# Performance work log

Measured on AMD Instinct MI355X. Metric: run time of the kernel, lower is better.

The kernel has to match this reference:

```python
import jax, jax.numpy as jnp
import numpy as np

N, M, FDIM, EDIM, H, HEADS = 8192, 8192, 128, 128, 64, 4
NEG = -1e9


def setup_inputs() -> dict:
    key = jax.random.key(0)
    ks = jax.random.split(key, 6)
    F0 = jax.random.normal(ks[0], (N, FDIM), dtype=jnp.float32)
    E0 = jax.random.normal(ks[1], (M, EDIM), dtype=jnp.float32)
    A = jax.random.randint(ks[2], (N, M), 0, 2, dtype=jnp.int32)
    Wf = jax.random.normal(ks[3], (HEADS, FDIM, H), dtype=jnp.float32) * 0.05
    We = jax.random.normal(ks[4], (HEADS, EDIM, H), dtype=jnp.float32) * 0.05
    a = jax.random.normal(ks[5], (HEADS, H), dtype=jnp.float32) * 0.05
    return {"F0": F0, "E0": E0, "A": A, "Wf": Wf, "We": We, "a": a}


def reference(F0, E0, A, Wf, We, a):
    # Per-head linear projections: h=head, n/m=nodes, d=hidden
    F1 = jnp.einsum('nf,hfd->hnd', F0, Wf)   # [H, N, D]
    E1 = jnp.einsum('me,hed->hmd', E0, We)   # [H, M, D]
    # Additive GAT scores: (h_src @ a) + (h_dst @ a), broadcast over the grid
    e_src = jnp.einsum('hnd,hd->hn', F1, a)  # [H, N]
    e_dst = jnp.einsum('hmd,hd->hm', E1, a)  # [H, M]
    e = jax.nn.leaky_relu(e_src[:, :, None] + e_dst[:, None, :], negative_slope=0.2)
    e = jnp.where(A[None, :, :] > 0, e, NEG)
    alpha = jax.nn.softmax(e, axis=-1)       # [H, N, M]
    h_prime = jnp.einsum('hnm,hmd->hnd', alpha, E1)  # [H, N, D]
    out = jnp.mean(h_prime, axis=0)          # mean over heads -> [N, D]
    return jax.nn.softmax(out, axis=-1)
```

## Files before the change

kernel.cpp:

```cpp
#include <hip/hip_runtime.h>
#include <hip/hip_fp16.h>

#define NN 8192
#define MM 8192
#define FD 128
#define EDm 128
#define HD 64
#define NH 4

#define MSPLIT 4
#define MRANGE (MM / MSPLIT)
#define MSTEP 128
#define NITER (MRANGE / MSTEP)
#define NTILE 32
#define AMS 132

typedef float f32x4 __attribute__((ext_vector_type(4)));
typedef _Float16 h16x8 __attribute__((ext_vector_type(8)));
typedef _Float16 h16x4 __attribute__((ext_vector_type(4)));
typedef __fp16 fp16x2 __attribute__((ext_vector_type(2)));

__device__ __forceinline__ float wmask(float edv, float ed2v, int a,
                                       float es, float es2, float esi) {
  float p = (edv > esi) ? es * edv : es2 * ed2v;
  return (a > 0) ? p : 0.0f;
}

__global__ void k_vf(const float* __restrict__ Wf, const float* __restrict__ a,
                     float* __restrict__ vf) {
  int t = threadIdx.x;
  int h = t >> 7, f = t & 127;
  const float* w = Wf + (size_t)(h * FD + f) * HD;
  const float* av = a + h * HD;
  float s = 0.f;
#pragma unroll
  for (int d = 0; d < HD; ++d) s += w[d] * av[d];
  vf[h * FD + f] = s;
}

__global__ void k_esrc(const float* __restrict__ F0, const float* __restrict__ vf,
                       float* __restrict__ esrc) {
  int t = blockIdx.x * blockDim.x + threadIdx.x;
  int n = t >> 2, h = t & 3;
  const float4* fr = (const float4*)(F0 + (size_t)n * FD);
  const float4* vr = (const float4*)(vf + h * FD);
  float s = 0.f;
#pragma unroll
  for (int i = 0; i < FD / 4; ++i) {
    float4 x = fr[i], y = vr[i];
    s += x.x * y.x + x.y * y.y + x.z * y.z + x.w * y.w;
  }
  esrc[h * NN + n] = s;
}

__global__ void k_e1(const float* __restrict__ E0, const float* __restrict__ We,
                     const float* __restrict__ a, _Float16* __restrict__ E1T,
                     float* __restrict__ ed, float* __restrict__ ed2) {
  int wid = (blockIdx.x * blockDim.x + threadIdx.x) >> 6;
  int lane = threadIdx.x & 63;
  int h = wid >> 11;
  int mg = wid & 2047;
  int m = mg * 4;
  const float* we = We + (size_t)h * EDm * HD + lane;
  const float* e0r = E0 + (size_t)m * EDm;
  float a0 = 0.f, a1 = 0.f, a2 = 0.f, a3 = 0.f;
#pragma unroll 4
  for (int e = 0; e < EDm; ++e) {
    float wv = we[e * HD];
    a0 += e0r[e] * wv;
    a1 += e0r[EDm + e] * wv;
    a2 += e0r[2 * EDm + e] * wv;
    a3 += e0r[3 * EDm + e] * wv;
  }
  h16x4 hv = {(_Float16)a0, (_Float16)a1, (_Float16)a2, (_Float16)a3};
  *(h16x4*)(E1T + (size_t)(h * HD + lane) * MM + m) = hv;
  float av = a[h * HD + lane];
  float d0 = a0 * av, d1 = a1 * av, d2 = a2 * av, d3 = a3 * av;
#pragma unroll
  for (int o = 32; o; o >>= 1) {
    d0 += __shfl_xor(d0, o);
    d1 += __shfl_xor(d1, o);
    d2 += __shfl_xor(d2, o);
    d3 += __shfl_xor(d3, o);
  }
  if (lane == 0) {
    const float L2E = 1.4426950408889634f;
    ed[h * MM + m + 0] = exp2f(d0 * L2E);
    ed[h * MM + m + 1] = exp2f(d1 * L2E);
    ed[h * MM + m + 2] = exp2f(d2 * L2E);
    ed[h * MM + m + 3] = exp2f(d3 * L2E);
    ed2[h * MM + m + 0] = exp2f(0.2f * d0 * L2E);
    ed2[h * MM + m + 1] = exp2f(0.2f * d1 * L2E);
    ed2[h * MM + m + 2] = exp2f(0.2f * d2 * L2E);
    ed2[h * MM + m + 3] = exp2f(0.2f * d3 * L2E);
  }
}

__global__ __launch_bounds__(256, 3) void k_main(
    const int* __restrict__ A, const _Float16* __restrict__ E1T,
    const float* __restrict__ esrc, const float* __restrict__ ed,
    const float* __restrict__ ed2, float* __restrict__ pnum,
    float* __restrict__ pden) {
  __shared__ int Am[NTILE * AMS];
  __shared__ float Ed[NH * 256];

  const int t = threadIdx.x;
  const int lane = t & 63;
  const int h = t >> 6;
  const int col = lane & 15;
  const int quad = lane >> 4;

  const int b = blockIdx.x;
  const int xcdr = b & 7;
  const int split = xcdr >> 1;
  const int ntile = ((b >> 3) << 1) | (xcdr & 1);
  const int n0 = ntile * NTILE;
  const int m0 = split * MRANGE;
  const float L2E = 1.4426950408889634f;

  float s0 = esrc[h * NN + n0 + col];
  float s1 = esrc[h * NN + n0 + 16 + col];
  float es0 = exp2f(s0 * L2E), eq0 = exp2f(0.2f * s0 * L2E), ei0 = exp2f(-s0 * L2E);
  float es1 = exp2f(s1 * L2E), eq1 = exp2f(0.2f * s1 * L2E), ei1 = exp2f(-s1 * L2E);

  f32x4 acc[2][4] = {};
  f32x4 accd[2] = {};
  const h16x8 ones = {(_Float16)1.f, (_Float16)1.f, (_Float16)1.f, (_Float16)1.f,
                      (_Float16)1.f, (_Float16)1.f, (_Float16)1.f, (_Float16)1.f};

  const int arow = t >> 3;
  const int achk = t & 7;
  const int* aptr = A + (size_t)(n0 + arow) * MM + m0 + achk * 4;
  int* amw = Am + arow * AMS + achk * 4;
  const float* edsrc = ((lane < 32) ? ed : ed2) + (size_t)h * MM + m0 + (lane & 31) * 4;
  float* edw = Ed + h * 256 + (lane >> 5) * 128 + (lane & 31) * 4;

  int4 apf[4];
#pragma unroll
  for (int j = 0; j < 4; ++j) apf[j] = *(const int4*)(aptr + 32 * j);
  float4 edpf = *(const float4*)edsrc;

  const _Float16* bq = E1T + (size_t)(h * HD + col) * MM + m0 + quad * 8;

  for (int it = 0; it < NITER; ++it) {
    const int k0 = it * MSTEP;
#pragma unroll
    for (int j = 0; j < 4; ++j) *(int4*)(amw + 32 * j) = apf[j];
    *(float4*)edw = edpf;
    __syncthreads();

    if (it + 1 < NITER) {
#pragma unroll
      for (int j = 0; j < 4; ++j)
        apf[j] = *(const int4*)(aptr + k0 + MSTEP + 32 * j);
      edpf = *(const float4*)(edsrc + k0 + MSTEP);
    }

#pragma unroll
    for (int kk = 0; kk < 4; ++kk) {
      const int kb = kk * 32 + quad * 8;
      const int* am0 = Am + col * AMS + kb;
      const int* am1 = Am + (col + 16) * AMS + kb;
      int4 ma0 = *(const int4*)am0;
      int4 ma1 = *(const int4*)(am0 + 4);
      int4 mb0 = *(const int4*)am1;
      int4 mb1 = *(const int4*)(am1 + 4);
      const float* ep = Ed + h * 256 + kb;
      f32x4 e0 = *(const f32x4*)ep;
      f32x4 e1 = *(const f32x4*)(ep + 4);
      f32x4 f0 = *(const f32x4*)(ep + 128);
      f32x4 f1 = *(const f32x4*)(ep + 132);

      union { h16x8 v; fp16x2 p[4]; } af0, af1;
      af0.p[0] = __builtin_amdgcn_cvt_pkrtz(wmask(e0[0], f0[0], ma0.x, es0, eq0, ei0),
                                            wmask(e0[1], f0[1], ma0.y, es0, eq0, ei0));
      af0.p[1] = __builtin_amdgcn_cvt_pkrtz(wmask(e0[2], f0[2], ma0.z, es0, eq0, ei0),
                                            wmask(e0[3], f0[3], ma0.w, es0, eq0, ei0));
      af0.p[2] = __builtin_amdgcn_cvt_pkrtz(wmask(e1[0], f1[0], ma1.x, es0, eq0, ei0),
                                            wmask(e1[1], f1[1], ma1.y, es0, eq0, ei0));
      af0.p[3] = __builtin_amdgcn_cvt_pkrtz(wmask(e1[2], f1[2], ma1.z, es0, eq0, ei0),
                                            wmask(e1[3], f1[3], ma1.w, es0, eq0, ei0));
      af1.p[0] = __builtin_amdgcn_cvt_pkrtz(wmask(e0[0], f0[0], mb0.x, es1, eq1, ei1),
                                            wmask(e0[1], f0[1], mb0.y, es1, eq1, ei1));
      af1.p[1] = __builtin_amdgcn_cvt_pkrtz(wmask(e0[2], f0[2], mb0.z, es1, eq1, ei1),
                                            wmask(e0[3], f0[3], mb0.w, es1, eq1, ei1));
      af1.p[2] = __builtin_amdgcn_cvt_pkrtz(wmask(e1[0], f1[0], mb1.x, es1, eq1, ei1),
                                            wmask(e1[1], f1[1], mb1.y, es1, eq1, ei1));
      af1.p[3] = __builtin_amdgcn_cvt_pkrtz(wmask(e1[2], f1[2], mb1.z, es1, eq1, ei1),
                                            wmask(e1[3], f1[3], mb1.w, es1, eq1, ei1));

#pragma unroll
      for (int dt = 0; dt < 4; ++dt) {
        h16x8 bfr = *(const h16x8*)(bq + (size_t)dt * 16 * MM + k0 + kk * 32);
        acc[0][dt] = __builtin_amdgcn_mfma_f32_16x16x32_f16(af0.v, bfr, acc[0][dt], 0, 0, 0);
        acc[1][dt] = __builtin_amdgcn_mfma_f32_16x16x32_f16(af1.v, bfr, acc[1][dt], 0, 0, 0);
      }
      accd[0] = __builtin_amdgcn_mfma_f32_16x16x32_f16(af0.v, ones, accd[0], 0, 0, 0);
      accd[1] = __builtin_amdgcn_mfma_f32_16x16x32_f16(af1.v, ones, accd[1], 0, 0, 0);
    }
    __syncthreads();
  }

  float* pn = pnum + (size_t)(split * NH + h) * NN * HD;
#pragma unroll
  for (int rt = 0; rt < 2; ++rt) {
#pragma unroll
    for (int dt = 0; dt < 4; ++dt) {
#pragma unroll
      for (int r2 = 0; r2 < 4; ++r2) {
        int n = n0 + rt * 16 + quad * 4 + r2;
        pn[(size_t)n * HD + dt * 16 + col] = acc[rt][dt][r2];
      }
    }
  }
  if (col == 0) {
    float* pd = pden + (size_t)(split * NH + h) * NN;
#pragma unroll
    for (int rt = 0; rt < 2; ++rt) {
#pragma unroll
      for (int r2 = 0; r2 < 4; ++r2)
        pd[n0 + rt * 16 + quad * 4 + r2] = accd[rt][r2];
    }
  }
}

__global__ void k_comb(const float* __restrict__ pnum, const float* __restrict__ pden,
                       float* __restrict__ out) {
  int t = threadIdx.x;
  int lane = t & 63, w = t >> 6;
  int n = blockIdx.x * 4 + w;
  float v = 0.f;
#pragma unroll
  for (int h = 0; h < NH; ++h) {
    float num = 0.f, den = 0.f;
#pragma unroll
    for (int s = 0; s < MSPLIT; ++s) {
      num += pnum[((size_t)(s * NH + h) * NN + n) * HD + lane];
      den += pden[(size_t)(s * NH + h) * NN + n];
    }
    v += num / den;
  }
  v *= 0.25f;
  float mx = v;
#pragma unroll
  for (int o = 32; o; o >>= 1) mx = fmaxf(mx, __shfl_xor(mx, o));
  const float L2E = 1.4426950408889634f;
  float p = exp2f((v - mx) * L2E);
  float sm = p;
#pragma unroll
  for (int o = 32; o; o >>= 1) sm += __shfl_xor(sm, o);
  out[(size_t)n * HD + lane] = p / sm;
}

extern "C" void kernel_launch(void* const* d_in, const int* in_sizes, int n_in,
                              void* d_out, int out_size, void* d_ws, size_t ws_size,
                              hipStream_t stream) {
  const float* F0 = (const float*)d_in[0];
  const float* E0 = (const float*)d_in[1];
  const int* A = (const int*)d_in[2];
  const float* Wf = (const float*)d_in[3];
  const float* We = (const float*)d_in[4];
  const float* a = (const float*)d_in[5];
  float* out = (float*)d_out;

  char* w = (char*)d_ws;
  float* esrc = (float*)w;       w += (size_t)NH * NN * 4;
  float* ed = (float*)w;         w += (size_t)NH * MM * 4;
  float* ed2 = (float*)w;        w += (size_t)NH * MM * 4;
  float* vf = (float*)w;         w += (size_t)NH * FD * 4;
  _Float16* E1T = (_Float16*)w;  w += (size_t)NH * HD * MM * 2;
  float* pnum = (float*)w;       w += (size_t)MSPLIT * NH * NN * HD * 4;
  float* pden = (float*)w;       w += (size_t)MSPLIT * NH * NN * 4;

  k_vf<<<1, 512, 0, stream>>>(Wf, a, vf);
  k_esrc<<<(NH * NN) / 256, 256, 0, stream>>>(F0, vf, esrc);
  k_e1<<<(NH * MM / 4) / 4, 256, 0, stream>>>(E0, We, a, E1T, ed, ed2);
  k_main<<<256 * MSPLIT, 256, 0, stream>>>(A, E1T, esrc, ed, ed2, pnum, pden);
  k_comb<<<NN / 4, 256, 0, stream>>>(pnum, pden, out);
}
```

Before: 554.8 us.

## Compute attention weights in packed fp16 with bitmask adjacency and staged output

The weight computation moves to packed fp16 vector math. max(ed*exp(0.8*es), ed2) rescales the leaky-relu exponent by a per-row constant exp(-0.2*es), which cancels in the softmax ratio. The adjacency tile is stored in shared memory as 16-bit AND masks instead of ints, and ed/ed2 are kept in fp16 to halve shared and global traffic. All 16 B-fragments are loaded into registers up front, A is read with nontemporal loads, and partial outputs are staged through shared memory for coalesced nontemporal stores. This raises register pressure (the occupancy hint of 3 is dropped) and risks fp16 overflow or underflow of the exponentials.

```diff
diff --git a/kernel.cpp b/kernel.cpp
--- a/kernel.cpp
+++ b/kernel.cpp
@@ -13,18 +13,12 @@
 #define MSTEP 128
 #define NITER (MRANGE / MSTEP)
 #define NTILE 32
-#define AMS 132
 
 typedef float f32x4 __attribute__((ext_vector_type(4)));
 typedef _Float16 h16x8 __attribute__((ext_vector_type(8)));
 typedef _Float16 h16x4 __attribute__((ext_vector_type(4)));
-typedef __fp16 fp16x2 __attribute__((ext_vector_type(2)));
-
-__device__ __forceinline__ float wmask(float edv, float ed2v, int a,
-                                       float es, float es2, float esi) {
-  float p = (edv > esi) ? es * edv : es2 * ed2v;
-  return (a > 0) ? p : 0.0f;
-}
+typedef int i32x4 __attribute__((ext_vector_type(4)));
+typedef unsigned int u32;
 
 __global__ void k_vf(const float* __restrict__ Wf, const float* __restrict__ a,
                      float* __restrict__ vf) {
@@ -55,7 +49,7 @@
 
 __global__ void k_e1(const float* __restrict__ E0, const float* __restrict__ We,
                      const float* __restrict__ a, _Float16* __restrict__ E1T,
-                     float* __restrict__ ed, float* __restrict__ ed2) {
+                     _Float16* __restrict__ edh, _Float16* __restrict__ ed2h) {
   int wid = (blockIdx.x * blockDim.x + threadIdx.x) >> 6;
   int lane = threadIdx.x & 63;
   int h = wid >> 11;
@@ -85,24 +79,33 @@
   }
   if (lane == 0) {
     const float L2E = 1.4426950408889634f;
-    ed[h * MM + m + 0] = exp2f(d0 * L2E);
-    ed[h * MM + m + 1] = exp2f(d1 * L2E);
-    ed[h * MM + m + 2] = exp2f(d2 * L2E);
-    ed[h * MM + m + 3] = exp2f(d3 * L2E);
-    ed2[h * MM + m + 0] = exp2f(0.2f * d0 * L2E);
-    ed2[h * MM + m + 1] = exp2f(0.2f * d1 * L2E);
-    ed2[h * MM + m + 2] = exp2f(0.2f * d2 * L2E);
-    ed2[h * MM + m + 3] = exp2f(0.2f * d3 * L2E);
-  }
-}
-
-__global__ __launch_bounds__(256, 3) void k_main(
+    edh[h * MM + m + 0] = (_Float16)exp2f(d0 * L2E);
+    edh[h * MM + m + 1] = (_Float16)exp2f(d1 * L2E);
+    edh[h * MM + m + 2] = (_Float16)exp2f(d2 * L2E);
+    edh[h * MM + m + 3] = (_Float16)exp2f(d3 * L2E);
+    ed2h[h * MM + m + 0] = (_Float16)exp2f(0.2f * d0 * L2E);
+    ed2h[h * MM + m + 1] = (_Float16)exp2f(0.2f * d1 * L2E);
+    ed2h[h * MM + m + 2] = (_Float16)exp2f(0.2f * d2 * L2E);
+    ed2h[h * MM + m + 3] = (_Float16)exp2f(0.2f * d3 * L2E);
+  }
+}
+
+__device__ __forceinline__ uint2 packmask(i32x4 a) {
+  uint2 r;
+  r.x = (a.x > 0 ? 0xffffu : 0u) | (a.y > 0 ? 0xffff0000u : 0u);
+  r.y = (a.z > 0 ? 0xffffu : 0u) | (a.w > 0 ? 0xffff0000u : 0u);
+  return r;
+}
+
+__global__ __launch_bounds__(256) void k_main(
     const int* __restrict__ A, const _Float16* __restrict__ E1T,
-    const float* __restrict__ esrc, const float* __restrict__ ed,
-    const float* __restrict__ ed2, float* __restrict__ pnum,
+    const float* __restrict__ esrc, const _Float16* __restrict__ edh,
+    const _Float16* __restrict__ ed2h, float* __restrict__ pnum,
     float* __restrict__ pden) {
-  __shared__ int Am[NTILE * AMS];
-  __shared__ float Ed[NH * 256];
+  __shared__ __align__(16) char smem[17408];
+  u32* Amh = (u32*)smem;
+  u32* EdU = (u32*)(smem + 8704);
+  float* Hpf = (float*)smem;
 
   const int t = threadIdx.x;
   const int lane = t & 63;
@@ -120,8 +123,10 @@
 
   float s0 = esrc[h * NN + n0 + col];
   float s1 = esrc[h * NN + n0 + 16 + col];
-  float es0 = exp2f(s0 * L2E), eq0 = exp2f(0.2f * s0 * L2E), ei0 = exp2f(-s0 * L2E);
-  float es1 = exp2f(s1 * L2E), eq1 = exp2f(0.2f * s1 * L2E), ei1 = exp2f(-s1 * L2E);
+  _Float16 e80 = (_Float16)exp2f(0.8f * s0 * L2E);
+  _Float16 e81 = (_Float16)exp2f(0.8f * s1 * L2E);
+  h16x8 es80 = {e80, e80, e80, e80, e80, e80, e80, e80};
+  h16x8 es81 = {e81, e81, e81, e81, e81, e81, e81, e81};
 
   f32x4 acc[2][4] = {};
   f32x4 accd[2] = {};
@@ -131,96 +136,93 @@
   const int arow = t >> 3;
   const int achk = t & 7;
   const int* aptr = A + (size_t)(n0 + arow) * MM + m0 + achk * 4;
-  int* amw = Am + arow * AMS + achk * 4;
-  const float* edsrc = ((lane < 32) ? ed : ed2) + (size_t)h * MM + m0 + (lane & 31) * 4;
-  float* edw = Ed + h * 256 + (lane >> 5) * 128 + (lane & 31) * 4;
-
-  int4 apf[4];
-#pragma unroll
-  for (int j = 0; j < 4; ++j) apf[j] = *(const int4*)(aptr + 32 * j);
-  float4 edpf = *(const float4*)edsrc;
+  u32* amw = Amh + arow * 68 + achk * 2;
+  const _Float16* edlane =
+      ((lane < 32) ? edh : ed2h) + (size_t)h * MM + m0 + (lane & 31) * 4;
+  u32* edw = EdU + h * 136 + ((lane >= 32) ? 68 : 0) + (lane & 31) * 2;
+
+  i32x4 apf[4];
+#pragma unroll
+  for (int j = 0; j < 4; ++j)
+    apf[j] = __builtin_nontemporal_load((const i32x4*)(aptr + 32 * j));
+  uint2 edpf = *(const uint2*)edlane;
 
   const _Float16* bq = E1T + (size_t)(h * HD + col) * MM + m0 + quad * 8;
 
   for (int it = 0; it < NITER; ++it) {
     const int k0 = it * MSTEP;
 #pragma unroll
-    for (int j = 0; j < 4; ++j) *(int4*)(amw + 32 * j) = apf[j];
-    *(float4*)edw = edpf;
-    __syncthreads();
+    for (int j = 0; j < 4; ++j) *(uint2*)(amw + 16 * j) = packmask(apf[j]);
+    *(uint2*)edw = edpf;
+    __syncthreads();
+
+    h16x8 bfr[16];
+#pragma unroll
+    for (int dt = 0; dt < 4; ++dt)
+#pragma unroll
+      for (int kk = 0; kk < 4; ++kk)
+        bfr[dt * 4 + kk] =
+            *(const h16x8*)(bq + (size_t)dt * 16 * MM + k0 + kk * 32);
 
     if (it + 1 < NITER) {
 #pragma unroll
       for (int j = 0; j < 4; ++j)
-        apf[j] = *(const int4*)(aptr + k0 + MSTEP + 32 * j);
-      edpf = *(const float4*)(edsrc + k0 + MSTEP);
+        apf[j] = __builtin_nontemporal_load(
+            (const i32x4*)(aptr + k0 + MSTEP + 32 * j));
+      edpf = *(const uint2*)(edlane + k0 + MSTEP);
     }
 
 #pragma unroll
     for (int kk = 0; kk < 4; ++kk) {
-      const int kb = kk * 32 + quad * 8;
-      const int* am0 = Am + col * AMS + kb;
-      const int* am1 = Am + (col + 16) * AMS + kb;
-      int4 ma0 = *(const int4*)am0;
-      int4 ma1 = *(const int4*)(am0 + 4);
-      int4 mb0 = *(const int4*)am1;
-      int4 mb1 = *(const int4*)(am1 + 4);
-      const float* ep = Ed + h * 256 + kb;
-      f32x4 e0 = *(const f32x4*)ep;
-      f32x4 e1 = *(const f32x4*)(ep + 4);
-      f32x4 f0 = *(const f32x4*)(ep + 128);
-      f32x4 f1 = *(const f32x4*)(ep + 132);
-
-      union { h16x8 v; fp16x2 p[4]; } af0, af1;
-      af0.p[0] = __builtin_amdgcn_cvt_pkrtz(wmask(e0[0], f0[0], ma0.x, es0, eq0, ei0),
-                                            wmask(e0[1], f0[1], ma0.y, es0, eq0, ei0));
-      af0.p[1] = __builtin_amdgcn_cvt_pkrtz(wmask(e0[2], f0[2], ma0.z, es0, eq0, ei0),
-                                            wmask(e0[3], f0[3], ma0.w, es0, eq0, ei0));
-      af0.p[2] = __builtin_amdgcn_cvt_pkrtz(wmask(e1[0], f1[0], ma1.x, es0, eq0, ei0),
-                                            wmask(e1[1], f1[1], ma1.y, es0, eq0, ei0));
-      af0.p[3] = __builtin_amdgcn_cvt_pkrtz(wmask(e1[2], f1[2], ma1.z, es0, eq0, ei0),
-                                            wmask(e1[3], f1[3], ma1.w, es0, eq0, ei0));
-      af1.p[0] = __builtin_amdgcn_cvt_pkrtz(wmask(e0[0], f0[0], mb0.x, es1, eq1, ei1),
-                                            wmask(e0[1], f0[1], mb0.y, es1, eq1, ei1));
-      af1.p[1] = __builtin_amdgcn_cvt_pkrtz(wmask(e0[2], f0[2], mb0.z, es1, eq1, ei1),
-                                            wmask(e0[3], f0[3], mb0.w, es1, eq1, ei1));
-      af1.p[2] = __builtin_amdgcn_cvt_pkrtz(wmask(e1[0], f1[0], mb1.x, es1, eq1, ei1),
-                                            wmask(e1[1], f1[1], mb1.y, es1, eq1, ei1));
-      af1.p[3] = __builtin_amdgcn_cvt_pkrtz(wmask(e1[2], f1[2], mb1.z, es1, eq1, ei1),
-                                            wmask(e1[3], f1[3], mb1.w, es1, eq1, ei1));
-
+      const int base = kk * 16 + quad * 4;
+      uint4 ma = *(const uint4*)(Amh + col * 68 + base);
+      uint4 mb = *(const uint4*)(Amh + (col + 16) * 68 + base);
+      h16x8 edv = *(const h16x8*)(EdU + h * 136 + base);
+      h16x8 e2v = *(const h16x8*)(EdU + h * 136 + 68 + base);
+      h16x8 w0 = __builtin_elementwise_max(edv * es80, e2v);
+      h16x8 w1 = __builtin_elementwise_max(edv * es81, e2v);
+      union { h16x8 v; uint4 u; } a0, a1;
+      a0.v = w0; a1.v = w1;
+      a0.u.x &= ma.x; a0.u.y &= ma.y; a0.u.z &= ma.z; a0.u.w &= ma.w;
+      a1.u.x &= mb.x; a1.u.y &= mb.y; a1.u.z &= mb.z; a1.u.w &= mb.w;
 #pragma unroll
       for (int dt = 0; dt < 4; ++dt) {
-        h16x8 bfr = *(const h16x8*)(bq + (size_t)dt * 16 * MM + k0 + kk * 32);
-        acc[0][dt] = __builtin_amdgcn_mfma_f32_16x16x32_f16(af0.v, bfr, acc[0][dt], 0, 0, 0);
-        acc[1][dt] = __builtin_amdgcn_mfma_f32_16x16x32_f16(af1.v, bfr, acc[1][dt], 0, 0, 0);
+        acc[0][dt] = __builtin_amdgcn_mfma_f32_16x16x32_f16(a0.v, bfr[dt * 4 + kk],
+                                                            acc[0][dt], 0, 0, 0);
+        acc[1][dt] = __builtin_amdgcn_mfma_f32_16x16x32_f16(a1.v, bfr[dt * 4 + kk],
+                                                            acc[1][dt], 0, 0, 0);
       }
-      accd[0] = __builtin_amdgcn_mfma_f32_16x16x32_f16(af0.v, ones, accd[0], 0, 0, 0);
-      accd[1] = __builtin_amdgcn_mfma_f32_16x16x32_f16(af1.v, ones, accd[1], 0, 0, 0);
+      accd[0] = __builtin_amdgcn_mfma_f32_16x16x32_f16(a0.v, ones, accd[0], 0, 0, 0);
+      accd[1] = __builtin_amdgcn_mfma_f32_16x16x32_f16(a1.v, ones, accd[1], 0, 0, 0);
     }
     __syncthreads();
   }
 
   float* pn = pnum + (size_t)(split * NH + h) * NN * HD;
+  float* pd = pden + (size_t)(split * NH + h) * NN;
 #pragma unroll
   for (int rt = 0; rt < 2; ++rt) {
 #pragma unroll
-    for (int dt = 0; dt < 4; ++dt) {
-#pragma unroll
-      for (int r2 = 0; r2 < 4; ++r2) {
-        int n = n0 + rt * 16 + quad * 4 + r2;
-        pn[(size_t)n * HD + dt * 16 + col] = acc[rt][dt][r2];
-      }
-    }
-  }
-  if (col == 0) {
-    float* pd = pden + (size_t)(split * NH + h) * NN;
-#pragma unroll
-    for (int rt = 0; rt < 2; ++rt) {
+    for (int dt = 0; dt < 4; ++dt)
 #pragma unroll
       for (int r2 = 0; r2 < 4; ++r2)
-        pd[n0 + rt * 16 + quad * 4 + r2] = accd[rt][r2];
-    }
+        Hpf[h * 1088 + (quad * 4 + r2) * 68 + dt * 16 + col] = acc[rt][dt][r2];
+    if (col == 0) {
+#pragma unroll
+      for (int r2 = 0; r2 < 4; ++r2)
+        Hpf[h * 1088 + (quad * 4 + r2) * 68 + 64] = accd[rt][r2];
+    }
+    __syncthreads();
+#pragma unroll
+    for (int j = 0; j < 4; ++j) {
+      int row = j * 4 + (lane >> 4);
+      int c4 = lane & 15;
+      f32x4 v = *(const f32x4*)(Hpf + h * 1088 + row * 68 + c4 * 4);
+      __builtin_nontemporal_store(
+          v, (f32x4*)(pn + (size_t)(n0 + rt * 16 + row) * HD + c4 * 4));
+    }
+    if (lane < 16) pd[n0 + rt * 16 + lane] = Hpf[h * 1088 + lane * 68 + 64];
+    __syncthreads();
   }
 }
 
@@ -264,17 +266,17 @@
   float* out = (float*)d_out;
 
   char* w = (char*)d_ws;
-  float* esrc = (float*)w;       w += (size_t)NH * NN * 4;
-  float* ed = (float*)w;         w += (size_t)NH * MM * 4;
-  float* ed2 = (float*)w;        w += (size_t)NH * MM * 4;
-  float* vf = (float*)w;         w += (size_t)NH * FD * 4;
-  _Float16* E1T = (_Float16*)w;  w += (size_t)NH * HD * MM * 2;
-  float* pnum = (float*)w;       w += (size_t)MSPLIT * NH * NN * HD * 4;
-  float* pden = (float*)w;       w += (size_t)MSPLIT * NH * NN * 4;
+  float* esrc = (float*)w;        w += (size_t)NH * NN * 4;
+  _Float16* edh = (_Float16*)w;   w += (size_t)NH * MM * 2;
+  _Float16* ed2h = (_Float16*)w;  w += (size_t)NH * MM * 2;
+  float* vf = (float*)w;          w += (size_t)NH * FD * 4;
+  _Float16* E1T = (_Float16*)w;   w += (size_t)NH * HD * MM * 2;
+  float* pnum = (float*)w;        w += (size_t)MSPLIT * NH * NN * HD * 4;
+  float* pden = (float*)w;        w += (size_t)MSPLIT * NH * NN * 4;
 
   k_vf<<<1, 512, 0, stream>>>(Wf, a, vf);
   k_esrc<<<(NH * NN) / 256, 256, 0, stream>>>(F0, vf, esrc);
-  k_e1<<<(NH * MM / 4) / 4, 256, 0, stream>>>(E0, We, a, E1T, ed, ed2);
-  k_main<<<256 * MSPLIT, 256, 0, stream>>>(A, E1T, esrc, ed, ed2, pnum, pden);
+  k_e1<<<(NH * MM / 4) / 4, 256, 0, stream>>>(E0, We, a, E1T, edh, ed2h);
+  k_main<<<256 * MSPLIT, 256, 0, stream>>>(A, E1T, esrc, edh, ed2h, pnum, pden);
   k_comb<<<NN / 4, 256, 0, stream>>>(pnum, pden, out);
 }
```

Result: faster. 518.4 us (-6.6%).
